# Performance work log

Hardware: AMD Instinct MI355X
Metric: run time of the kernel (lower is better)

Reference implementation:

```python
import jax, jax.numpy as jnp
import numpy as np

B, IN_DIM, EMB, D_NUM, M_NUM, TAU = 32768, 768, 768, 9, 10, 32.0


def setup_inputs() -> dict:
    key = jax.random.key(0)
    k1, k2, k3, k4, k5 = jax.random.split(key, 5)
    feature = jax.random.normal(k1, (B, IN_DIM), dtype=jnp.float32)
    category = jax.random.randint(k2, (B,), 0, D_NUM, dtype=jnp.int64)
    # nn.Linear(input_dim, emb_dim, bias=False) weights: [emb_dim, input_dim]
    s = 1.0 / np.sqrt(IN_DIM)
    W_topic = jax.random.uniform(k3, (EMB, IN_DIM), jnp.float32, -s, s)
    W_domain = jax.random.uniform(k4, (EMB, IN_DIM), jnp.float32, -s, s)
    # stacked per-domain memory banks: [domain_num, memory_num, emb_dim]
    domain_memory = jax.random.normal(k5, (D_NUM, M_NUM, EMB), dtype=jnp.float32)
    return {"feature": feature, "category": category, "W_topic": W_topic,
            "W_domain": W_domain, "domain_memory": domain_memory}


def reference(feature, category, W_topic, W_domain, domain_memory):
    # norm(x): L2-normalize each row
    length = jnp.sqrt(jnp.sum(feature * feature, axis=1, keepdims=True))
    feature = feature / length
    q_topic = feature @ W_topic.T   # [B, EMB]
    q_dom = feature @ W_domain.T    # [B, EMB]
    # per-domain attention over memory bank, batched over domains
    scores = jnp.einsum('be,dme->bdm', q_topic, domain_memory) * TAU
    topic_att = jax.nn.softmax(scores, axis=-1)                 # [B, D, M]
    sep_emb = jnp.einsum('bdm,dme->bde', topic_att, domain_memory)  # [B, D, EMB]
    domain_att = jnp.einsum('bde,be->bd', sep_emb, q_dom) * TAU
    domain_att = jax.nn.softmax(domain_att, axis=1)[:, None, :]  # [B, 1, D]
    return domain_att
```

## Files before the change

### kernel.cpp

```cpp
#include <hip/hip_runtime.h>
#include <hip/hip_fp8.h>
#include <math.h>

#define TAU 32.0f
#define LO_SCALE 2048.0f
#define INV_LO_SCALE (1.0f/2048.0f)

typedef _Float16 f16x8 __attribute__((ext_vector_type(8)));
typedef _Float16 f16x4 __attribute__((ext_vector_type(4)));
typedef __fp16   fp16v2 __attribute__((ext_vector_type(2)));
typedef float    f32x2 __attribute__((ext_vector_type(2)));
typedef float    f32x16 __attribute__((ext_vector_type(16)));

#if defined(__has_builtin)
#if __has_builtin(__builtin_amdgcn_cvt_f32_fp8) && __has_builtin(__builtin_amdgcn_cvt_pk_fp8_f32)
#define HAVE_FP8_BUILTINS 1
#endif
#if __has_builtin(__builtin_amdgcn_cvt_pk_f32_fp8) && __has_builtin(__builtin_amdgcn_cvt_pkrtz)
#define HAVE_FP8_PK 1
#endif
#endif

static __device__ __forceinline__ unsigned char enc_e4m3(float x) {
#ifdef HAVE_FP8_BUILTINS
    int p = __builtin_amdgcn_cvt_pk_fp8_f32(x, x, 0, false);
    return (unsigned char)(p & 0xff);
#else
    __hip_fp8_e4m3 q(x);
    return (unsigned char)q.__x;
#endif
}

#ifdef HAVE_FP8_BUILTINS
#define DEC_E4M3(W, SEL) __builtin_amdgcn_cvt_f32_fp8((int)(W), (SEL))
#else
static __device__ __forceinline__ float dec_e4m3_sw(unsigned w, int sel) {
    __hip_fp8_e4m3 q; q.__x = (unsigned char)((w >> (8 * sel)) & 0xff);
    return (float)q;
}
#define DEC_E4M3(W, SEL) dec_e4m3_sw((W), (SEL))
#endif

static __device__ __forceinline__ f16x8 dec8(uint2 w) {
    f16x8 r;
#ifdef HAVE_FP8_PK
    f32x2 a = __builtin_amdgcn_cvt_pk_f32_fp8((int)w.x, false);
    f32x2 b = __builtin_amdgcn_cvt_pk_f32_fp8((int)w.x, true);
    f32x2 c = __builtin_amdgcn_cvt_pk_f32_fp8((int)w.y, false);
    f32x2 d = __builtin_amdgcn_cvt_pk_f32_fp8((int)w.y, true);
    fp16v2 h0 = __builtin_amdgcn_cvt_pkrtz(a[0], a[1]);
    fp16v2 h1 = __builtin_amdgcn_cvt_pkrtz(b[0], b[1]);
    fp16v2 h2 = __builtin_amdgcn_cvt_pkrtz(c[0], c[1]);
    fp16v2 h3 = __builtin_amdgcn_cvt_pkrtz(d[0], d[1]);
    r[0] = (_Float16)h0[0]; r[1] = (_Float16)h0[1];
    r[2] = (_Float16)h1[0]; r[3] = (_Float16)h1[1];
    r[4] = (_Float16)h2[0]; r[5] = (_Float16)h2[1];
    r[6] = (_Float16)h3[0]; r[7] = (_Float16)h3[1];
#else
    r[0] = (_Float16)DEC_E4M3(w.x, 0); r[1] = (_Float16)DEC_E4M3(w.x, 1);
    r[2] = (_Float16)DEC_E4M3(w.x, 2); r[3] = (_Float16)DEC_E4M3(w.x, 3);
    r[4] = (_Float16)DEC_E4M3(w.y, 0); r[5] = (_Float16)DEC_E4M3(w.y, 1);
    r[6] = (_Float16)DEC_E4M3(w.y, 2); r[7] = (_Float16)DEC_E4M3(w.y, 3);
#endif
    return r;
}

__global__ __launch_bounds__(1024) void precompute_mw_packed(
    const float* __restrict__ Wt, const float* __restrict__ Wd,
    const float* __restrict__ dmem, _Float16* __restrict__ PBhi,
    unsigned char* __restrict__ PBlo)
{
    __shared__ float Ml[3 * 768];
    __shared__ float red[3][4][256];
    const int nt  = blockIdx.x;
    const int kc  = blockIdx.y;
    const int n0  = nt * 3;
    const int tid = threadIdx.x;
    const int q   = tid >> 8;
    const int kl  = tid & 255;
    const int k   = kc * 256 + kl;
    float v[3] = {0.f, 0.f, 0.f};
    if (n0 < 180) {
        const float* __restrict__ W = (n0 < 90) ? Wt : Wd;
        const int m0 = (n0 < 90) ? n0 : n0 - 90;
        for (int idx = tid; idx < 3 * 768; idx += 1024)
            Ml[idx] = dmem[m0 * 768 + idx];
        __syncthreads();
        const float* __restrict__ Wq  = W + (q * 192) * 768 + k;
        const float* __restrict__ mlb = Ml + q * 192;
        float a0 = 0.f, a1 = 0.f, a2 = 0.f;
        for (int e0 = 0; e0 < 192; e0 += 8) {
            float w[8];
            #pragma unroll
            for (int i = 0; i < 8; ++i)
                w[i] = Wq[(e0 + i) * 768];
            float4 m0a = *(const float4*)(mlb + e0);
            float4 m0b = *(const float4*)(mlb + e0 + 4);
            float4 m1a = *(const float4*)(mlb + 768 + e0);
            float4 m1b = *(const float4*)(mlb + 768 + e0 + 4);
            float4 m2a = *(const float4*)(mlb + 1536 + e0);
            float4 m2b = *(const float4*)(mlb + 1536 + e0 + 4);
            a0 = fmaf(m0a.x, w[0], a0); a0 = fmaf(m0a.y, w[1], a0);
            a0 = fmaf(m0a.z, w[2], a0); a0 = fmaf(m0a.w, w[3], a0);
            a0 = fmaf(m0b.x, w[4], a0); a0 = fmaf(m0b.y, w[5], a0);
            a0 = fmaf(m0b.z, w[6], a0); a0 = fmaf(m0b.w, w[7], a0);
            a1 = fmaf(m1a.x, w[0], a1); a1 = fmaf(m1a.y, w[1], a1);
            a1 = fmaf(m1a.z, w[2], a1); a1 = fmaf(m1a.w, w[3], a1);
            a1 = fmaf(m1b.x, w[4], a1); a1 = fmaf(m1b.y, w[5], a1);
            a1 = fmaf(m1b.z, w[6], a1); a1 = fmaf(m1b.w, w[7], a1);
            a2 = fmaf(m2a.x, w[0], a2); a2 = fmaf(m2a.y, w[1], a2);
            a2 = fmaf(m2a.z, w[2], a2); a2 = fmaf(m2a.w, w[3], a2);
            a2 = fmaf(m2b.x, w[4], a2); a2 = fmaf(m2b.y, w[5], a2);
            a2 = fmaf(m2b.z, w[6], a2); a2 = fmaf(m2b.w, w[7], a2);
        }
        red[0][q][kl] = a0;
        red[1][q][kl] = a1;
        red[2][q][kl] = a2;
        __syncthreads();
        if (q == 0) {
            #pragma unroll
            for (int i = 0; i < 3; ++i)
                v[i] = red[i][0][kl] + red[i][1][kl] + red[i][2][kl] + red[i][3][kl];
        }
    }
    if (q == 0) {
        const int t = k >> 5, ks = (k >> 4) & 1, h = (k >> 3) & 1, j = k & 7;
        const int fragc = (t * 2 + ks) * 6;
        #pragma unroll
        for (int i = 0; i < 3; ++i) {
            const int n = n0 + i;
            const int idx = (fragc + (n >> 5)) * 512 + (h * 32 + (n & 31)) * 8 + j;
            _Float16 hi = (_Float16)v[i];
            float lo = (v[i] - (float)hi) * LO_SCALE;
            PBhi[idx] = hi;
            PBlo[idx] = enc_e4m3(lo);
        }
    }
}

#define LOADB2(S, KL) do {                                   \
    Bh##S = *(const f16x8*)(pbh + (KL) * 3072);              \
    Bl##S = *(const uint2*)(pbl + (KL) * 3072);              \
} while (0)

#define CONV4(P, BUF) do {                                   \
    float _xs[4] = {(P).x, (P).y, (P).z, (P).w};             \
    f16x4 _h, _l;                                            \
    _Pragma("unroll")                                        \
    for (int _i = 0; _i < 4; ++_i) {                         \
        float _x = _xs[_i];                                  \
        _Float16 _hh = (_Float16)_x;                         \
        _h[_i] = _hh;                                        \
        _l[_i] = (_Float16)((_x - (float)_hh) * LO_SCALE);   \
        ps += _x * _x;                                       \
    }                                                        \
    *(f16x4*)((char*)AhL[BUF] + wb) = _h;                    \
    *(f16x4*)((char*)AlL[BUF] + wb) = _l;                    \
} while (0)

#define MBODY(BUF, KS, BH, BL) do {                          \
    const int _ao = (arow * 64 + (KS) * 32 + asel) ^ swzA;   \
    f16x8 _ah = *(const f16x8*)((const char*)AhL[BUF] + _ao);\
    f16x8 _al = *(const f16x8*)((const char*)AlL[BUF] + _ao);\
    f16x8 _bl = dec8(BL);                                    \
    acc1 = __builtin_amdgcn_mfma_f32_32x32x16_f16(_ah, BH, acc1, 0, 0, 0);  \
    acc2 = __builtin_amdgcn_mfma_f32_32x32x16_f16(_ah, _bl, acc2, 0, 0, 0); \
    acc2 = __builtin_amdgcn_mfma_f32_32x32x16_f16(_al, BH, acc2, 0, 0, 0);  \
} while (0)

__global__ __launch_bounds__(384) void fused_memnet(
    const float* __restrict__ F, const _Float16* __restrict__ PBhi,
    const unsigned char* __restrict__ PBlo, float* __restrict__ out)
{
    __shared__ alignas(16) _Float16 AhL[2][32 * 32];
    __shared__ alignas(16) _Float16 AlL[2][32 * 32];
    __shared__ float raw[32 * 196];
    __shared__ float ss[32];

    const int tid  = threadIdx.x;
    const int lane = tid & 63;
    const int wid  = tid / 64;
    const int row0 = blockIdx.x * 32;

    const int srow = (tid >> 3) & 31;
    const int sc4  = tid & 7;
    const float* __restrict__ Fp = F + (row0 + srow) * 768 + sc4 * 4;
    const int wb = (srow * 64 + sc4 * 8) ^ ((srow & 7) << 4);

    const _Float16*      __restrict__ pbh = PBhi + wid * 512 + lane * 8;
    const unsigned char* __restrict__ pbl = PBlo + wid * 512 + lane * 8;

    const int arow = lane & 31;
    const int swzA = (arow & 7) << 4;
    const int asel = (lane >> 5) * 16;

    f32x16 acc1, acc2;
    #pragma unroll
    for (int r = 0; r < 16; ++r) { acc1[r] = 0.f; acc2[r] = 0.f; }

    float ps = 0.f;
    float4 p00, ppA, ppB;
    f16x8 Bh0, Bh1, Bh2, Bh3;
    uint2 Bl0, Bl1, Bl2, Bl3;

    if (tid < 256) {
        p00 = *(const float4*)(Fp);
        ppA = *(const float4*)(Fp + 32);
        ppB = *(const float4*)(Fp + 64);
        CONV4(p00, 0);
    }
    LOADB2(0, 0);
    LOADB2(1, 1);
    __syncthreads();

    for (int th = 0; th < 24; th += 2) {
        if (th < 23) { LOADB2(2, 2 * th + 2); LOADB2(3, 2 * th + 3); }
        MBODY(0, 0, Bh0, Bl0);
        if (tid < 256 && th < 23) CONV4(ppA, 1);
        if (tid < 256 && th < 21) ppA = *(const float4*)(Fp + (th + 3) * 32);
        MBODY(0, 1, Bh1, Bl1);
        __syncthreads();
        const int T1 = th + 1;
        if (T1 < 23) { LOADB2(0, 2 * T1 + 2); LOADB2(1, 2 * T1 + 3); }
        MBODY(1, 0, Bh2, Bl2);
        if (tid < 256 && T1 < 23) CONV4(ppB, 0);
        if (tid < 256 && T1 < 21) ppB = *(const float4*)(Fp + (T1 + 3) * 32);
        MBODY(1, 1, Bh3, Bl3);
        __syncthreads();
    }

    if (tid < 256) {
        ps += __shfl_xor(ps, 1); ps += __shfl_xor(ps, 2); ps += __shfl_xor(ps, 4);
        if (sc4 == 0) ss[srow] = ps;
    }

    #pragma unroll
    for (int r = 0; r < 16; ++r) {
        const int rl = (r & 3) + 8 * (r >> 2) + 4 * (lane >> 5);
        raw[rl * 196 + wid * 32 + (lane & 31)] = acc1[r] + acc2[r] * INV_LO_SCALE;
    }
    __syncthreads();

    if (tid < 32) {
        const int r = tid;
        const float s = TAU / sqrtf(ss[r]);
        const float* Sr = raw + r * 196;
        float logit[9];
        #pragma unroll
        for (int d = 0; d < 9; ++d) {
            float vv[10];
            float mx = -1e30f;
            #pragma unroll
            for (int m = 0; m < 10; ++m) {
                vv[m] = s * Sr[d * 10 + m];
                mx = fmaxf(mx, vv[m]);
            }
            float den = 0.f, num = 0.f;
            #pragma unroll
            for (int m = 0; m < 10; ++m) {
                const float e = expf(vv[m] - mx);
                den += e;
                num = fmaf(e, Sr[90 + d * 10 + m], num);
            }
            logit[d] = s * num / den;
        }
        float mx2 = -1e30f;
        #pragma unroll
        for (int d = 0; d < 9; ++d) mx2 = fmaxf(mx2, logit[d]);
        float e2[9], den2 = 0.f;
        #pragma unroll
        for (int d = 0; d < 9; ++d) { e2[d] = expf(logit[d] - mx2); den2 += e2[d]; }
        const float inv = 1.f / den2;
        float* op = out + (row0 + r) * 9;
        #pragma unroll
        for (int d = 0; d < 9; ++d) op[d] = e2[d] * inv;
    }
}

extern "C" void kernel_launch(void* const* d_in, const int* in_sizes, int n_in,
                              void* d_out, int out_size, void* d_ws, size_t ws_size,
                              hipStream_t stream)
{
    const float* feature = (const float*)d_in[0];
    const float* Wt   = (const float*)d_in[2];
    const float* Wd   = (const float*)d_in[3];
    const float* dmem = (const float*)d_in[4];
    float* outp = (float*)d_out;
    _Float16* PBhi = (_Float16*)d_ws;
    unsigned char* PBlo = (unsigned char*)d_ws + 192 * 768 * 2;

    precompute_mw_packed<<<dim3(64, 3), 1024, 0, stream>>>(Wt, Wd, dmem, PBhi, PBlo);
    fused_memnet<<<32768 / 32, 384, 0, stream>>>(feature, PBhi, PBlo, outp);
}
```

Baseline: 66.10 us.

## Load A fragments directly from global into registers, dropping LDS staging and barriers

```diff
diff --git a/kernel.cpp b/kernel.cpp
--- a/kernel.cpp
+++ b/kernel.cpp
@@ -7,7 +7,6 @@
 #define INV_LO_SCALE (1.0f/2048.0f)
 
 typedef _Float16 f16x8 __attribute__((ext_vector_type(8)));
-typedef _Float16 f16x4 __attribute__((ext_vector_type(4)));
 typedef __fp16   fp16v2 __attribute__((ext_vector_type(2)));
 typedef float    f32x2 __attribute__((ext_vector_type(2)));
 typedef float    f32x16 __attribute__((ext_vector_type(16)));
@@ -138,42 +137,23 @@
     }
 }
 
-#define LOADB2(S, KL) do {                                   \
-    Bh##S = *(const f16x8*)(pbh + (KL) * 3072);              \
-    Bl##S = *(const uint2*)(pbl + (KL) * 3072);              \
-} while (0)
-
-#define CONV4(P, BUF) do {                                   \
-    float _xs[4] = {(P).x, (P).y, (P).z, (P).w};             \
-    f16x4 _h, _l;                                            \
+#define CONVA(X0, X1, AH, AL) do {                           \
+    float _xs[8] = {(X0).x, (X0).y, (X0).z, (X0).w,          \
+                    (X1).x, (X1).y, (X1).z, (X1).w};         \
     _Pragma("unroll")                                        \
-    for (int _i = 0; _i < 4; ++_i) {                         \
+    for (int _i = 0; _i < 8; ++_i) {                         \
         float _x = _xs[_i];                                  \
         _Float16 _hh = (_Float16)_x;                         \
-        _h[_i] = _hh;                                        \
-        _l[_i] = (_Float16)((_x - (float)_hh) * LO_SCALE);   \
+        AH[_i] = _hh;                                        \
+        AL[_i] = (_Float16)((_x - (float)_hh) * LO_SCALE);   \
         ps += _x * _x;                                       \
     }                                                        \
-    *(f16x4*)((char*)AhL[BUF] + wb) = _h;                    \
-    *(f16x4*)((char*)AlL[BUF] + wb) = _l;                    \
-} while (0)
-
-#define MBODY(BUF, KS, BH, BL) do {                          \
-    const int _ao = (arow * 64 + (KS) * 32 + asel) ^ swzA;   \
-    f16x8 _ah = *(const f16x8*)((const char*)AhL[BUF] + _ao);\
-    f16x8 _al = *(const f16x8*)((const char*)AlL[BUF] + _ao);\
-    f16x8 _bl = dec8(BL);                                    \
-    acc1 = __builtin_amdgcn_mfma_f32_32x32x16_f16(_ah, BH, acc1, 0, 0, 0);  \
-    acc2 = __builtin_amdgcn_mfma_f32_32x32x16_f16(_ah, _bl, acc2, 0, 0, 0); \
-    acc2 = __builtin_amdgcn_mfma_f32_32x32x16_f16(_al, BH, acc2, 0, 0, 0);  \
 } while (0)
 
 __global__ __launch_bounds__(384) void fused_memnet(
     const float* __restrict__ F, const _Float16* __restrict__ PBhi,
     const unsigned char* __restrict__ PBlo, float* __restrict__ out)
 {
-    __shared__ alignas(16) _Float16 AhL[2][32 * 32];
-    __shared__ alignas(16) _Float16 AlL[2][32 * 32];
     __shared__ float raw[32 * 196];
     __shared__ float ss[32];
 
@@ -182,57 +162,47 @@
     const int wid  = tid / 64;
     const int row0 = blockIdx.x * 32;
 
-    const int srow = (tid >> 3) & 31;
-    const int sc4  = tid & 7;
-    const float* __restrict__ Fp = F + (row0 + srow) * 768 + sc4 * 4;
-    const int wb = (srow * 64 + sc4 * 8) ^ ((srow & 7) << 4);
+    const int arow = lane & 31;
+    const float* __restrict__ Fp = F + (row0 + arow) * 768 + (lane >> 5) * 8;
 
     const _Float16*      __restrict__ pbh = PBhi + wid * 512 + lane * 8;
     const unsigned char* __restrict__ pbl = PBlo + wid * 512 + lane * 8;
-
-    const int arow = lane & 31;
-    const int swzA = (arow & 7) << 4;
-    const int asel = (lane >> 5) * 16;
 
     f32x16 acc1, acc2;
     #pragma unroll
     for (int r = 0; r < 16; ++r) { acc1[r] = 0.f; acc2[r] = 0.f; }
 
     float ps = 0.f;
-    float4 p00, ppA, ppB;
-    f16x8 Bh0, Bh1, Bh2, Bh3;
-    uint2 Bl0, Bl1, Bl2, Bl3;
-
-    if (tid < 256) {
-        p00 = *(const float4*)(Fp);
-        ppA = *(const float4*)(Fp + 32);
-        ppB = *(const float4*)(Fp + 64);
-        CONV4(p00, 0);
-    }
-    LOADB2(0, 0);
-    LOADB2(1, 1);
-    __syncthreads();
-
-    for (int th = 0; th < 24; th += 2) {
-        if (th < 23) { LOADB2(2, 2 * th + 2); LOADB2(3, 2 * th + 3); }
-        MBODY(0, 0, Bh0, Bl0);
-        if (tid < 256 && th < 23) CONV4(ppA, 1);
-        if (tid < 256 && th < 21) ppA = *(const float4*)(Fp + (th + 3) * 32);
-        MBODY(0, 1, Bh1, Bl1);
-        __syncthreads();
-        const int T1 = th + 1;
-        if (T1 < 23) { LOADB2(0, 2 * T1 + 2); LOADB2(1, 2 * T1 + 3); }
-        MBODY(1, 0, Bh2, Bl2);
-        if (tid < 256 && T1 < 23) CONV4(ppB, 0);
-        if (tid < 256 && T1 < 21) ppB = *(const float4*)(Fp + (T1 + 3) * 32);
-        MBODY(1, 1, Bh3, Bl3);
-        __syncthreads();
-    }
-
-    if (tid < 256) {
-        ps += __shfl_xor(ps, 1); ps += __shfl_xor(ps, 2); ps += __shfl_xor(ps, 4);
-        if (sc4 == 0) ss[srow] = ps;
-    }
+
+    #pragma unroll 2
+    for (int t = 0; t < 24; ++t) {
+        const float* __restrict__ fw = Fp + t * 32;
+        float4 x0 = *(const float4*)(fw);
+        float4 x1 = *(const float4*)(fw + 4);
+        float4 x2 = *(const float4*)(fw + 16);
+        float4 x3 = *(const float4*)(fw + 20);
+        f16x8 bh0 = *(const f16x8*)(pbh + (2 * t) * 3072);
+        uint2 bw0 = *(const uint2*)(pbl + (2 * t) * 3072);
+        f16x8 bh1 = *(const f16x8*)(pbh + (2 * t + 1) * 3072);
+        uint2 bw1 = *(const uint2*)(pbl + (2 * t + 1) * 3072);
+
+        f16x8 ah0, al0;
+        CONVA(x0, x1, ah0, al0);
+        f16x8 bl0 = dec8(bw0);
+        acc1 = __builtin_amdgcn_mfma_f32_32x32x16_f16(ah0, bh0, acc1, 0, 0, 0);
+        acc2 = __builtin_amdgcn_mfma_f32_32x32x16_f16(ah0, bl0, acc2, 0, 0, 0);
+        acc2 = __builtin_amdgcn_mfma_f32_32x32x16_f16(al0, bh0, acc2, 0, 0, 0);
+
+        f16x8 ah1, al1;
+        CONVA(x2, x3, ah1, al1);
+        f16x8 bl1 = dec8(bw1);
+        acc1 = __builtin_amdgcn_mfma_f32_32x32x16_f16(ah1, bh1, acc1, 0, 0, 0);
+        acc2 = __builtin_amdgcn_mfma_f32_32x32x16_f16(ah1, bl1, acc2, 0, 0, 0);
+        acc2 = __builtin_amdgcn_mfma_f32_32x32x16_f16(al1, bh1, acc2, 0, 0, 0);
+    }
+
+    ps += __shfl_xor(ps, 32);
+    if (tid < 32) ss[tid] = ps;
 
     #pragma unroll
     for (int r = 0; r < 16; ++r) {
```

Result: slower. 112.9 us (+70.8%).
